# Performance work log

Hardware: AMD Instinct MI355X
Metric: run time of the kernel (lower is better)

## Reference

```python
import jax, jax.numpy as jnp
import numpy as np


def setup_inputs() -> dict:
    key = jax.random.key(0)
    kq, kk, kv = jax.random.split(key, 3)
    B, S, D = 8, 2048, 128
    Q = jax.random.normal(kq, (B, S, D), dtype=jnp.float32)
    K = jax.random.normal(kk, (B, S, D), dtype=jnp.float32)
    V = jax.random.normal(kv, (B, S, D), dtype=jnp.float32)
    return {"Q": Q, "K": K, "V": V}


def reference(Q, K, V):
    # scores: [B, S, S]
    d = Q.shape[-1]
    scores = jnp.einsum('bqd,bkd->bqk', Q, K) / jnp.sqrt(jnp.float32(d))
    # causal mask: position i attends to keys <= i (original sets upper triangle to -inf)
    S = scores.shape[-1]
    causal = jnp.tril(jnp.ones((S, S), dtype=bool))  # [S, S]
    scores = jnp.where(causal[None, :, :], scores, -jnp.inf)
    probs = jax.nn.softmax(scores, axis=-1)
    return jnp.einsum('bqk,bkd->bqd', probs, V)
```

## Files before the change

### kernel.cpp

```cpp
#include <hip/hip_runtime.h>

#define BB 8
#define SS 2048
#define DD 128
#define SEG ((size_t)BB * SS * DD)

typedef _Float16 f16;
typedef _Float16 f16x2 __attribute__((ext_vector_type(2)));
typedef __fp16 h16x2 __attribute__((ext_vector_type(2)));
typedef _Float16 f16x8 __attribute__((ext_vector_type(8)));
typedef float f32x4 __attribute__((ext_vector_type(4)));
typedef int i32x4 __attribute__((ext_vector_type(4)));

#define SWV(d) ((((d) & 7) ^ (((d) >> 3) & 7)) << 3)

#define DEFER_THR 4.0f

static __device__ __forceinline__ float fast_exp2(float x) {
#if __has_builtin(__builtin_amdgcn_exp2f)
    return __builtin_amdgcn_exp2f(x);
#else
    return exp2f(x);
#endif
}

static __device__ __forceinline__ f16x2 cvt_pk(float a, float b) {
    h16x2 r = __builtin_amdgcn_cvt_pkrtz(a, b);
    return __builtin_bit_cast(f16x2, r);
}

static __device__ __forceinline__ int cvt_pk_i(float a, float b) {
    return __builtin_bit_cast(int, cvt_pk(a, b));
}

static __device__ __forceinline__ uint2 pack4(f32x4 v) {
    uint2 u;
    u.x = (unsigned)cvt_pk_i(v[0], v[1]);
    u.y = (unsigned)cvt_pk_i(v[2], v[3]);
    return u;
}

template <int NS>
__global__ __launch_bounds__(256, 2)
void attn_fwd(const float* __restrict__ Qg, const float* __restrict__ Kg,
              const float* __restrict__ Vg, float* __restrict__ Og,
              f16* __restrict__ Opf, float2* __restrict__ mlb)
{
    __shared__ __align__(16) f16 Kl[2][64 * 128];
    __shared__ __align__(16) f16 Vt[2][128 * 64];

    const int tid  = threadIdx.x;
    const int lane = tid & 63;
    const int w    = tid >> 6;
    const int c_   = lane & 15;
    const int g    = lane >> 4;

    const int L   = blockIdx.x;
    const int bb  = L & 7;
    const int rem = L >> 3;
    const int qb  = 31 - (rem / NS);
    const int sg  = rem % NS;
    const int T   = qb + 1;
    const int t0  = (T * sg) / NS;
    const int t1  = (T * (sg + 1)) / NS;

    const int qrow0 = qb * 64 + w * 16;
    const int qi    = qrow0 + c_;

    const int srcA = c_ + 32 * (g & 1);
    const int srcB = srcA + 16;
    const int selH = g >> 1;

    const float qs = 0.08838834764831845f * 1.4426950408889634f;
    f16x8 qf[4];
    {
        const float* qp = Qg + (size_t)(bb * SS + qi) * DD;
#pragma unroll
        for (int kk = 0; kk < 4; ++kk) {
            const int d0 = kk * 32 + g * 8;
            f32x4 a = *(const f32x4*)(qp + d0);
            f32x4 b = *(const f32x4*)(qp + d0 + 4);
            f16x8 q;
#pragma unroll
            for (int i = 0; i < 4; ++i) {
                q[i]     = (f16)(a[i] * qs);
                q[i + 4] = (f16)(b[i] * qs);
            }
            qf[kk] = q;
        }
    }

    f32x4 Oa[8];
#pragma unroll
    for (int i = 0; i < 8; ++i) Oa[i] = (f32x4){0.f, 0.f, 0.f, 0.f};
    float mrun  = -1e30f;
    float lpart = 0.f;

    const int krow = tid >> 5;
    const int kc4  = tid & 31;
    const int vkg  = tid >> 5;
    const int vq   = tid & 31;

    f32x4 kreg[8], vreg[8];

#define LOADT(tt)                                                              \
    {                                                                          \
        const size_t gb = (size_t)(bb * SS + (tt) * 64) * DD;                  \
        _Pragma("unroll")                                                      \
        for (int j = 0; j < 8; ++j)                                            \
            kreg[j] = *(const f32x4*)(Kg + gb + (krow + 8 * j) * DD + kc4 * 4);\
        _Pragma("unroll")                                                      \
        for (int i = 0; i < 8; ++i)                                            \
            vreg[i] = *(const f32x4*)(Vg + gb + (vkg * 8 + i) * DD + vq * 4);  \
    }

#define STAGE_K(pb_)                                                           \
    {                                                                          \
        _Pragma("unroll")                                                      \
        for (int j = 0; j < 8; ++j) {                                          \
            const int row = krow + 8 * j;                                      \
            const int el  = row * 128 + ((kc4 * 4) ^ ((row & 7) << 3));        \
            *(uint2*)&Kl[pb_][el] = pack4(kreg[j]);                            \
        }                                                                      \
    }

#define STAGE_V(pb_)                                                           \
    {                                                                          \
        _Pragma("unroll")                                                      \
        for (int dd = 0; dd < 4; ++dd) {                                       \
            const int d  = vq * 4 + dd;                                        \
            const int sw = SWV(d);                                             \
            _Pragma("unroll")                                                  \
            for (int h = 0; h < 2; ++h) {                                      \
                f32x4 vv = {vreg[4 * h + 0][dd], vreg[4 * h + 1][dd],          \
                            vreg[4 * h + 2][dd], vreg[4 * h + 3][dd]};         \
                const int el = d * 64 + ((vkg * 8 + 4 * h) ^ sw);              \
                *(uint2*)&Vt[pb_][el] = pack4(vv);                             \
            }                                                                  \
        }                                                                      \
    }

    if (t0 < t1) {
        LOADT(t0);
        STAGE_K(t0 & 1);
        STAGE_V(t0 & 1);
        if (t0 + 1 < t1) LOADT(t0 + 1);
        __syncthreads();

        for (int t = t0; t < t1; ++t) {
            const int pb = t & 1;
            const bool more = (t + 1 < t1);
            const int kbase = t * 64;

            f32x4 s4[4];
            __builtin_amdgcn_s_setprio(1);
#pragma unroll
            for (int nb = 0; nb < 4; ++nb) {
                f32x4 acc = (f32x4){0.f, 0.f, 0.f, 0.f};
                const int row = c_ + nb * 16;
                const int sw  = (row & 7) << 3;
#pragma unroll
                for (int kk = 0; kk < 4; ++kk) {
                    f16x8 kb = *(const f16x8*)&Kl[pb][row * 128 + ((kk * 32 + g * 8) ^ sw)];
                    acc = __builtin_amdgcn_mfma_f32_16x16x32_f16(kb, qf[kk], acc, 0, 0, 0);
                }
                s4[nb] = acc;
            }
            __builtin_amdgcn_s_setprio(0);

            if (more) STAGE_K(pb ^ 1);

            if (t == qb) {
#pragma unroll
                for (int nb = 0; nb < 4; ++nb)
#pragma unroll
                    for (int r = 0; r < 4; ++r) {
                        const int kj = kbase + nb * 16 + g * 4 + r;
                        if (kj > qi) s4[nb][r] = -1e30f;
                    }
            }

            float pm = -1e30f;
#pragma unroll
            for (int nb = 0; nb < 4; ++nb) {
                f32x4 v = s4[nb];
                pm = fmaxf(pm, fmaxf(fmaxf(v[0], v[1]), fmaxf(v[2], v[3])));
            }
            pm = fmaxf(pm, __shfl_xor(pm, 16));
            pm = fmaxf(pm, __shfl_xor(pm, 32));

            if (!__all(pm - mrun <= DEFER_THR)) {
                float sc;
                if (pm - mrun <= DEFER_THR) {
                    sc = 1.0f;
                } else {
                    sc = fast_exp2(mrun - pm);
                    mrun = pm;
                }
                lpart *= sc;
#pragma unroll
                for (int dblk = 0; dblk < 8; ++dblk) {
                    Oa[dblk][0] *= sc; Oa[dblk][1] *= sc;
                    Oa[dblk][2] *= sc; Oa[dblk][3] *= sc;
                }
            }

            int ph_lo[4], ph_hi[4];
#pragma unroll
            for (int nb = 0; nb < 4; ++nb) {
                float p0 = fast_exp2(s4[nb][0] - mrun);
                float p1 = fast_exp2(s4[nb][1] - mrun);
                float p2 = fast_exp2(s4[nb][2] - mrun);
                float p3 = fast_exp2(s4[nb][3] - mrun);
                lpart += (p0 + p1) + (p2 + p3);
                ph_lo[nb] = cvt_pk_i(p0, p1);
                ph_hi[nb] = cvt_pk_i(p2, p3);
            }

            if (more) STAGE_V(pb ^ 1);

#pragma unroll
            for (int ks = 0; ks < 2; ++ks) {
                const int lo1L = __shfl(ph_lo[2 * ks + 0], srcA);
                const int hi1L = __shfl(ph_hi[2 * ks + 0], srcA);
                const int lo2L = __shfl(ph_lo[2 * ks + 0], srcB);
                const int hi2L = __shfl(ph_hi[2 * ks + 0], srcB);
                const int lo1H = __shfl(ph_lo[2 * ks + 1], srcA);
                const int hi1H = __shfl(ph_hi[2 * ks + 1], srcA);
                const int lo2H = __shfl(ph_lo[2 * ks + 1], srcB);
                const int hi2H = __shfl(ph_hi[2 * ks + 1], srcB);
                i32x4 bw;
                bw[0] = selH ? lo1H : lo1L;
                bw[1] = selH ? hi1H : hi1L;
                bw[2] = selH ? lo2H : lo2L;
                bw[3] = selH ? hi2H : hi2L;
                const f16x8 pbfrag = __builtin_bit_cast(f16x8, bw);

                __builtin_amdgcn_s_setprio(1);
#pragma unroll
                for (int dblk = 0; dblk < 8; ++dblk) {
                    const int d  = dblk * 16 + c_;
                    f16x8 vb = *(const f16x8*)&Vt[pb][d * 64 + ((ks * 32 + g * 8) ^ SWV(d))];
                    Oa[dblk] = __builtin_amdgcn_mfma_f32_16x16x32_f16(vb, pbfrag, Oa[dblk], 0, 0, 0);
                }
                __builtin_amdgcn_s_setprio(0);
            }

            if (t + 2 < t1) LOADT(t + 2);
            if (more) __syncthreads();
        }
    }

    float lrun = lpart;
    lrun += __shfl_xor(lrun, 16);
    lrun += __shfl_xor(lrun, 32);

    if (NS == 1) {
        float* dst = Og + (size_t)(bb * SS + qi) * DD + g * 4;
        const float inv = (lrun > 0.f) ? 1.0f / lrun : 0.f;
#pragma unroll
        for (int dblk = 0; dblk < 8; ++dblk) {
            float4 o;
            o.x = Oa[dblk][0] * inv; o.y = Oa[dblk][1] * inv;
            o.z = Oa[dblk][2] * inv; o.w = Oa[dblk][3] * inv;
            *(float4*)(dst + dblk * 16) = o;
        }
    } else {
        f16* od = Opf + (size_t)sg * SEG + (size_t)(bb * SS + qi) * DD + g * 4;
#pragma unroll
        for (int dblk = 0; dblk < 8; ++dblk)
            *(uint2*)(od + dblk * 16) = pack4(Oa[dblk]);
        if (g == 0)
            mlb[(size_t)sg * BB * SS + bb * SS + qi] = make_float2(mrun, lrun);
    }
}

template <int NS>
__global__ __launch_bounds__(256)
void merge_kernel(float* __restrict__ out, const f16* __restrict__ Opf,
                  const float2* __restrict__ mlb)
{
    const int idx = blockIdx.x * 256 + threadIdx.x;
    const int row = idx >> 4;
    float2 ml[NS];
#pragma unroll
    for (int i = 0; i < NS; ++i) ml[i] = mlb[(size_t)i * BB * SS + row];
    float mm = ml[0].x;
#pragma unroll
    for (int i = 1; i < NS; ++i) mm = fmaxf(mm, ml[i].x);
    float e[NS], den = 0.f;
#pragma unroll
    for (int i = 0; i < NS; ++i) {
        e[i] = fast_exp2(ml[i].x - mm);
        den += ml[i].y * e[i];
    }
    const float inv = 1.0f / den;

    float acc[8] = {0.f, 0.f, 0.f, 0.f, 0.f, 0.f, 0.f, 0.f};
#pragma unroll
    for (int i = 0; i < NS; ++i) {
        f16x8 v = *(const f16x8*)(Opf + (size_t)i * SEG + (size_t)idx * 8);
#pragma unroll
        for (int j = 0; j < 8; ++j) acc[j] += (float)v[j] * e[i];
    }
    float4 o0, o1;
    o0.x = acc[0] * inv; o0.y = acc[1] * inv; o0.z = acc[2] * inv; o0.w = acc[3] * inv;
    o1.x = acc[4] * inv; o1.y = acc[5] * inv; o1.z = acc[6] * inv; o1.w = acc[7] * inv;
    float4* dst = (float4*)(out + (size_t)idx * 8);
    dst[0] = o0;
    dst[1] = o1;
}

extern "C" void kernel_launch(void* const* d_in, const int* in_sizes, int n_in,
                              void* d_out, int out_size, void* d_ws, size_t ws_size,
                              hipStream_t stream)
{
    const float* Q = (const float*)d_in[0];
    const float* K = (const float*)d_in[1];
    const float* V = (const float*)d_in[2];
    float* out = (float*)d_out;

    const size_t OPB = SEG * sizeof(f16);
    const size_t MLB = (size_t)BB * SS * sizeof(float2);
    const int mergeGrid = (int)(SEG / 8 / 256);

    const size_t need4 = 4 * OPB + 4 * MLB;

    if (ws_size >= need4) {
        f16*    Opf = (f16*)d_ws;
        float2* mlb = (float2*)((char*)d_ws + 4 * OPB);
        hipLaunchKernelGGL((attn_fwd<4>), dim3(8 * 32 * 4), dim3(256), 0, stream,
                           Q, K, V, out, Opf, mlb);
        hipLaunchKernelGGL((merge_kernel<4>), dim3(mergeGrid), dim3(256), 0, stream,
                           out, Opf, mlb);
    } else {
        hipLaunchKernelGGL((attn_fwd<1>), dim3(8 * 32), dim3(256), 0, stream,
                           Q, K, V, out, (f16*)nullptr, (float2*)nullptr);
    }
}
```

Measured before the change: 103.3 us.

## Permute K rows in LDS so P fragments feed PV MFMA without shuffles

K tile rows are stored in LDS under a permuted row order, chosen so that each lane's QK^T score outputs already sit in the positions the P·V MFMA B-operand expects. This removes the eight cross-lane shuffles and selects per k-step. The causal mask index is updated to match. K and V staging also switch to 16-byte LDS stores, with 8 fp16 values packed per store instead of 4, which lowers the LDS store instruction count. The risk is more bank conflicts from the new store pattern, and the mapping must be exactly right to stay correct.

```diff
diff --git a/kernel.cpp b/kernel.cpp
--- a/kernel.cpp
+++ b/kernel.cpp
@@ -31,13 +31,6 @@
 
 static __device__ __forceinline__ int cvt_pk_i(float a, float b) {
     return __builtin_bit_cast(int, cvt_pk(a, b));
-}
-
-static __device__ __forceinline__ uint2 pack4(f32x4 v) {
-    uint2 u;
-    u.x = (unsigned)cvt_pk_i(v[0], v[1]);
-    u.y = (unsigned)cvt_pk_i(v[2], v[3]);
-    return u;
 }
 
 template <int NS>
@@ -67,10 +60,6 @@
     const int qrow0 = qb * 64 + w * 16;
     const int qi    = qrow0 + c_;
 
-    const int srcA = c_ + 32 * (g & 1);
-    const int srcB = srcA + 16;
-    const int selH = g >> 1;
-
     const float qs = 0.08838834764831845f * 1.4426950408889634f;
     f16x8 qf[4];
     {
@@ -96,19 +85,22 @@
     float mrun  = -1e30f;
     float lpart = 0.f;
 
-    const int krow = tid >> 5;
-    const int kc4  = tid & 31;
+    const int kcg  = tid & 15;
+    const int krow = tid >> 4;
     const int vkg  = tid >> 5;
     const int vq   = tid & 31;
 
-    f32x4 kreg[8], vreg[8];
+    f32x4 kreg[4][2], vreg[8];
 
 #define LOADT(tt)                                                              \
     {                                                                          \
         const size_t gb = (size_t)(bb * SS + (tt) * 64) * DD;                  \
         _Pragma("unroll")                                                      \
-        for (int j = 0; j < 8; ++j)                                            \
-            kreg[j] = *(const f32x4*)(Kg + gb + (krow + 8 * j) * DD + kc4 * 4);\
+        for (int j = 0; j < 4; ++j) {                                          \
+            const float* kp = Kg + gb + (krow + 16 * j) * DD + kcg * 8;        \
+            kreg[j][0] = *(const f32x4*)(kp);                                  \
+            kreg[j][1] = *(const f32x4*)(kp + 4);                              \
+        }                                                                      \
         _Pragma("unroll")                                                      \
         for (int i = 0; i < 8; ++i)                                            \
             vreg[i] = *(const f32x4*)(Vg + gb + (vkg * 8 + i) * DD + vq * 4);  \
@@ -117,10 +109,17 @@
 #define STAGE_K(pb_)                                                           \
     {                                                                          \
         _Pragma("unroll")                                                      \
-        for (int j = 0; j < 8; ++j) {                                          \
-            const int row = krow + 8 * j;                                      \
-            const int el  = row * 128 + ((kc4 * 4) ^ ((row & 7) << 3));        \
-            *(uint2*)&Kl[pb_][el] = pack4(kreg[j]);                            \
+        for (int j = 0; j < 4; ++j) {                                          \
+            const int u  = krow + 16 * j;                                      \
+            const int Lr = (((u >> 5) & 1) + 2 * ((u >> 2) & 1)) * 16          \
+                         + ((u >> 3) & 3) * 4 + (u & 3);                       \
+            const int el = Lr * 128 + ((kcg * 8) ^ ((Lr & 7) << 3));           \
+            uint4 u4;                                                          \
+            u4.x = (unsigned)cvt_pk_i(kreg[j][0][0], kreg[j][0][1]);           \
+            u4.y = (unsigned)cvt_pk_i(kreg[j][0][2], kreg[j][0][3]);           \
+            u4.z = (unsigned)cvt_pk_i(kreg[j][1][0], kreg[j][1][1]);           \
+            u4.w = (unsigned)cvt_pk_i(kreg[j][1][2], kreg[j][1][3]);           \
+            *(uint4*)&Kl[pb_][el] = u4;                                        \
         }                                                                      \
     }
 
@@ -129,14 +128,13 @@
         _Pragma("unroll")                                                      \
         for (int dd = 0; dd < 4; ++dd) {                                       \
             const int d  = vq * 4 + dd;                                        \
-            const int sw = SWV(d);                                             \
-            _Pragma("unroll")                                                  \
-            for (int h = 0; h < 2; ++h) {                                      \
-                f32x4 vv = {vreg[4 * h + 0][dd], vreg[4 * h + 1][dd],          \
-                            vreg[4 * h + 2][dd], vreg[4 * h + 3][dd]};         \
-                const int el = d * 64 + ((vkg * 8 + 4 * h) ^ sw);              \
-                *(uint2*)&Vt[pb_][el] = pack4(vv);                             \
-            }                                                                  \
+            const int el = d * 64 + ((vkg * 8) ^ SWV(d));                      \
+            uint4 u4;                                                          \
+            u4.x = (unsigned)cvt_pk_i(vreg[0][dd], vreg[1][dd]);               \
+            u4.y = (unsigned)cvt_pk_i(vreg[2][dd], vreg[3][dd]);               \
+            u4.z = (unsigned)cvt_pk_i(vreg[4][dd], vreg[5][dd]);               \
+            u4.w = (unsigned)cvt_pk_i(vreg[6][dd], vreg[7][dd]);               \
+            *(uint4*)&Vt[pb_][el] = u4;                                        \
         }                                                                      \
     }
 
@@ -175,7 +173,7 @@
                 for (int nb = 0; nb < 4; ++nb)
 #pragma unroll
                     for (int r = 0; r < 4; ++r) {
-                        const int kj = kbase + nb * 16 + g * 4 + r;
+                        const int kj = kbase + 8 * g + 32 * (nb & 1) + 4 * (nb >> 1) + r;
                         if (kj > qi) s4[nb][r] = -1e30f;
                     }
             }
@@ -221,19 +219,11 @@
 
 #pragma unroll
             for (int ks = 0; ks < 2; ++ks) {
-                const int lo1L = __shfl(ph_lo[2 * ks + 0], srcA);
-                const int hi1L = __shfl(ph_hi[2 * ks + 0], srcA);
-                const int lo2L = __shfl(ph_lo[2 * ks + 0], srcB);
-                const int hi2L = __shfl(ph_hi[2 * ks + 0], srcB);
-                const int lo1H = __shfl(ph_lo[2 * ks + 1], srcA);
-                const int hi1H = __shfl(ph_hi[2 * ks + 1], srcA);
-                const int lo2H = __shfl(ph_lo[2 * ks + 1], srcB);
-                const int hi2H = __shfl(ph_hi[2 * ks + 1], srcB);
                 i32x4 bw;
-                bw[0] = selH ? lo1H : lo1L;
-                bw[1] = selH ? hi1H : hi1L;
-                bw[2] = selH ? lo2H : lo2L;
-                bw[3] = selH ? hi2H : hi2L;
+                bw[0] = ph_lo[ks];
+                bw[1] = ph_hi[ks];
+                bw[2] = ph_lo[ks + 2];
+                bw[3] = ph_hi[ks + 2];
                 const f16x8 pbfrag = __builtin_bit_cast(f16x8, bw);
 
                 __builtin_amdgcn_s_setprio(1);
@@ -268,8 +258,12 @@
     } else {
         f16* od = Opf + (size_t)sg * SEG + (size_t)(bb * SS + qi) * DD + g * 4;
 #pragma unroll
-        for (int dblk = 0; dblk < 8; ++dblk)
-            *(uint2*)(od + dblk * 16) = pack4(Oa[dblk]);
+        for (int dblk = 0; dblk < 8; ++dblk) {
+            uint2 u;
+            u.x = (unsigned)cvt_pk_i(Oa[dblk][0], Oa[dblk][1]);
+            u.y = (unsigned)cvt_pk_i(Oa[dblk][2], Oa[dblk][3]);
+            *(uint2*)(od + dblk * 16) = u;
+        }
         if (g == 0)
             mlb[(size_t)sg * BB * SS + bb * SS + qi] = make_float2(mrun, lrun);
     }
```

Measured after the change: 101.0 us. -2.3%, faster.
